# Optimization experiments

Measured on AMD Instinct MI355X. Metric: run time of the kernel, lower is better.

The kernel has to match this reference:

```python
import jax, jax.numpy as jnp
import numpy as np

D_MODEL = 1024
K_QUERY = 32
K_TOPK = 4

def setup_inputs() -> dict:
    key = jax.random.key(0)
    k1, k2, k3, k4, k5 = jax.random.split(key, 5)
    x = jax.random.normal(k1, (4, 2048, D_MODEL), dtype=jnp.float32)
    # nn.Linear(d_model, k_query): weight [k_query, d_model], bias [k_query]
    sc = 1.0 / np.sqrt(D_MODEL)
    Wq = jax.random.uniform(k2, (K_QUERY, D_MODEL), jnp.float32, -sc, sc)
    bq = jax.random.uniform(k3, (K_QUERY,), jnp.float32, -sc, sc)
    Wk = jax.random.uniform(k4, (K_QUERY, D_MODEL), jnp.float32, -sc, sc)
    bk = jax.random.uniform(k5, (K_QUERY,), jnp.float32, -sc, sc)
    return {"x": x, "Wq": Wq, "bq": bq, "Wk": Wk, "bk": bk}

def reference(x, Wq, bq, Wk, bk):
    # x: [B, T, D]
    queries = jnp.einsum('btd,kd->btk', x, Wq) + bq      # [B, T, Kq]
    keys = jnp.einsum('btd,kd->btk', x, Wk) + bk         # [B, T, Kq]
    sim = jnp.einsum('btk,bsk->bts', queries, keys)      # [B, T, T]
    sim = sim / jnp.sqrt(jnp.float32(queries.shape[-1]))
    _, topk_idx = jax.lax.top_k(sim, K_TOPK)              # [B, T, K]
    # gather neighbors per (b, t): x[b, topk_idx[b, t]] -> [B, T, K, D]
    neighbors = jax.vmap(lambda xb, ib: xb[ib])(x, topk_idx)
    gathered = neighbors.mean(axis=2)                     # [B, T, D]
    return gathered
```

## Files before the change

kernel.cpp:

```cpp
#include <hip/hip_runtime.h>
#include <math.h>

#define D_MODEL 1024
#define T_SEQ   2048
#define NBATCH  4
#define NROWS   (NBATCH * T_SEQ)
#define NOUT    64
#define NQTR    4

#define SKLD 264
#define SQLD 36
#define XLD  1032

typedef double v4df __attribute__((ext_vector_type(4)));

__device__ __forceinline__ bool key_gt(float av, int ai, float bv, int bi) {
    return (av > bv) || (av == bv && ai < bi);
}

__device__ __forceinline__ void cmpswap(float& v0, int& i0, float& v1, int& i1) {
    bool sw = key_gt(v1, i1, v0, i0);
    float nv0 = sw ? v1 : v0, nv1 = sw ? v0 : v1;
    int   ni0 = sw ? i1 : i0, ni1 = sw ? i0 : i1;
    v0 = nv0; v1 = nv1; i0 = ni0; i1 = ni1;
}

__device__ __forceinline__ void merge4(float (&a)[4], int (&ai)[4],
                                       float b0, int j0, float b1, int j1,
                                       float b2, int j2, float b3, int j3) {
    if (!key_gt(a[0], ai[0], b3, j3)) { a[0] = b3; ai[0] = j3; }
    if (!key_gt(a[1], ai[1], b2, j2)) { a[1] = b2; ai[1] = j2; }
    if (!key_gt(a[2], ai[2], b1, j1)) { a[2] = b1; ai[2] = j1; }
    if (!key_gt(a[3], ai[3], b0, j0)) { a[3] = b0; ai[3] = j0; }
    cmpswap(a[0], ai[0], a[2], ai[2]);
    cmpswap(a[1], ai[1], a[3], ai[3]);
    cmpswap(a[0], ai[0], a[1], ai[1]);
    cmpswap(a[2], ai[2], a[3], ai[3]);
}

__device__ __forceinline__ void insert4(float (&tv)[4], int (&tix)[4], float v, int idx) {
    if (v > tv[3]) {
        bool g0 = v > tv[0], g1 = v > tv[1], g2 = v > tv[2];
        float n0 = g0 ? v : tv[0];
        int   m0 = g0 ? idx : tix[0];
        float n1 = g1 ? (g0 ? tv[0] : v) : tv[1];
        int   m1 = g1 ? (g0 ? tix[0] : idx) : tix[1];
        float n2 = g2 ? (g1 ? tv[1] : v) : tv[2];
        int   m2 = g2 ? (g1 ? tix[1] : idx) : tix[2];
        float n3 = g2 ? tv[2] : v;
        int   m3 = g2 ? tix[2] : idx;
        tv[0] = n0; tv[1] = n1; tv[2] = n2; tv[3] = n3;
        tix[0] = m0; tix[1] = m1; tix[2] = m2; tix[3] = m3;
    }
}

__global__ __launch_bounds__(64) void mfma_probe(int* __restrict__ tab)
{
    __shared__ double Aref[16][4];
    __shared__ double Bref[4][16];
    __shared__ double Dref[16][16];

    const int lane = threadIdx.x;
    {
        const int m = lane & 15, k = lane >> 4;
        Aref[m][k] = (double)(1 + m * 4 + k);
        Bref[k][m] = (double)(1 + k * 16 + m);
    }
    __syncthreads();
    for (int e = lane; e < 256; e += 64) {
        const int m = e >> 4, n = e & 15;
        double s = 0.0;
        for (int k = 0; k < 4; ++k) s += Aref[m][k] * Bref[k][n];
        Dref[m][n] = s;
    }
    __syncthreads();

    int found = -1;
    for (int h = 0; h < 16; ++h) {
        if (found >= 0) break;
        const int fa = h & 1, fb = (h >> 1) & 1, fd = h >> 2;
        const int am = fa ? (lane >> 2) : (lane & 15);
        const int ak = fa ? (lane & 3)  : (lane >> 4);
        const int bn = fb ? (lane >> 2) : (lane & 15);
        const int bk = fb ? (lane & 3)  : (lane >> 4);
        v4df c = {0.0, 0.0, 0.0, 0.0};
        c = __builtin_amdgcn_mfma_f64_16x16x4f64(Aref[am][ak], Bref[bk][bn], c, 0, 0, 0);
        bool ok = true;
        #pragma unroll
        for (int i = 0; i < 4; ++i) {
            int dm, dn;
            if (fd == 0)      { dm = 4 * (lane >> 4) + i; dn = lane & 15; }
            else if (fd == 1) { dn = 4 * (lane >> 4) + i; dm = lane & 15; }
            else if (fd == 2) { dm = (lane >> 4) + 4 * i; dn = lane & 15; }
            else              { dn = (lane >> 4) + 4 * i; dm = lane & 15; }
            if (c[i] != Dref[dm][dn]) ok = false;
        }
        if (__all(ok)) found = h;
    }

    const int fa = (found >= 0) ? (found & 1) : 0;
    const int fb = (found >= 0) ? ((found >> 1) & 1) : 0;
    const int fd = (found >= 0) ? (found >> 2) : 0;
    tab[1   + lane] = fa ? (lane >> 2) : (lane & 15);
    tab[65  + lane] = fa ? (lane & 3)  : (lane >> 4);
    tab[129 + lane] = fb ? (lane & 3)  : (lane >> 4);
    tab[193 + lane] = fb ? (lane >> 2) : (lane & 15);
    #pragma unroll
    for (int i = 0; i < 4; ++i) {
        int dm, dn;
        if (fd == 0)      { dm = 4 * (lane >> 4) + i; dn = lane & 15; }
        else if (fd == 1) { dn = 4 * (lane >> 4) + i; dm = lane & 15; }
        else if (fd == 2) { dm = (lane >> 4) + 4 * i; dn = lane & 15; }
        else              { dn = (lane >> 4) + 4 * i; dm = lane & 15; }
        tab[257 + lane * 4 + i] = dm;
        tab[513 + lane * 4 + i] = dn;
    }
    if (lane == 0) tab[0] = found;
}

__global__ __launch_bounds__(256) void wprep_kernel(
    const float* __restrict__ Wq, const float* __restrict__ Wk,
    double* __restrict__ Wdt)
{
    const int idx = blockIdx.x * 256 + threadIdx.x;
    const int o = idx & 63;
    const int d = idx >> 6;
    float v = (o < 32) ? Wq[(size_t)o * D_MODEL + d]
                       : Wk[(size_t)(o - 32) * D_MODEL + d];
    Wdt[(size_t)d * 64 + o] = (double)v;
}

__global__ __launch_bounds__(512) void proj_mfma(
    const float* __restrict__ x, const double* __restrict__ Wdt,
    const float* __restrict__ bq, const float* __restrict__ bk_,
    const int* __restrict__ tab,
    float* __restrict__ Qt, float* __restrict__ Kt)
{
    __shared__ float  xlds[16 * XLD];
    __shared__ double comb[4][64][4];

    const int tid  = threadIdx.x;
    const int lane = tid & 63;
    const int wav  = tid >> 6;
    const int og   = __builtin_amdgcn_readfirstlane(wav >> 1);
    const int half = __builtin_amdgcn_readfirstlane(wav & 1);
    const int row0 = blockIdx.x * 16;
    const int dbase = half * 512;

    const int flag = tab[0];
    const int am  = tab[1   + lane];
    const int ak  = tab[65  + lane];
    const int bkk = tab[129 + lane];
    const int bn  = tab[193 + lane];

    const double* wcol = Wdt + og * 16;

    #pragma unroll
    for (int j = 0; j < 8; ++j) {
        const int f  = j * 512 + tid;
        const int r  = f >> 8;
        const int c4 = f & 255;
        float4 v = *reinterpret_cast<const float4*>(
            x + (size_t)(row0 + r) * D_MODEL + c4 * 4);
        *reinterpret_cast<float4*>(&xlds[r * XLD + c4 * 4]) = v;
    }
    __syncthreads();

    v4df acc = {0.0, 0.0, 0.0, 0.0};

    if (flag >= 0) {
        #pragma unroll 8
        for (int kk = 0; kk < 128; ++kk) {
            double a = (double)xlds[am * XLD + dbase + kk * 4 + ak];
            double b = wcol[(size_t)(dbase + kk * 4 + bkk) * 64 + bn];
            acc = __builtin_amdgcn_mfma_f64_16x16x4f64(a, b, acc, 0, 0, 0);
        }
    } else {
        const int n  = lane & 15;
        const int r4 = (lane >> 4) * 4;
        for (int dd = 0; dd < 512; ++dd) {
            const int d = dbase + dd;
            double wv = wcol[(size_t)d * 64 + n];
            #pragma unroll
            for (int i = 0; i < 4; ++i)
                acc[i] = fma((double)xlds[(r4 + i) * XLD + d], wv, acc[i]);
        }
    }

    if (half == 1) {
        #pragma unroll
        for (int i = 0; i < 4; ++i) comb[og][lane][i] = acc[i];
    }
    __syncthreads();

    if (half == 0) {
        #pragma unroll
        for (int i = 0; i < 4; ++i) {
            const double tot = acc[i] + comb[og][lane][i];
            const int dmv = tab[257 + lane * 4 + i];
            const int dnv = tab[513 + lane * 4 + i];
            const int out = og * 16 + dnv;
            const int row = row0 + dmv;
            const int bb  = row >> 11, t = row & 2047;
            const double bias = (out < 32) ? (double)bq[out] : (double)bk_[out - 32];
            const float v = (float)(tot + bias);
            if (out < 32) Qt[((size_t)bb * 32 + out) * T_SEQ + t] = v;
            else          Kt[((size_t)bb * 32 + (out - 32)) * T_SEQ + t] = v;
        }
    }
}

__global__ __launch_bounds__(256) void sim_topk(
    const float* __restrict__ Qt, const float* __restrict__ Kt,
    float* __restrict__ candVal ,
    int*   __restrict__ candIdx )
{
    __shared__ float klds[32 * SKLD];
    __shared__ float qlds[32 * SQLD];
    __shared__ float cV[4][32][4];
    __shared__ int   cI[4][32][4];

    const int tid  = threadIdx.x;
    const int lane = tid & 63;
    const int wav  = tid >> 6;
    const int qtr  = blockIdx.x & 3;
    const int tt   = (blockIdx.x >> 2) & 63;
    const int b    = blockIdx.x >> 8;
    const int tblk = tt * 32;
    const int sq0  = qtr * 512;

    const float* QtB = Qt + (size_t)b * 32 * T_SEQ;
    const float* KtB = Kt + (size_t)b * 32 * T_SEQ;

    {
        const int i  = tid >> 3;
        const int t4 = (tid & 7) * 4;
        float4 v = *reinterpret_cast<const float4*>(QtB + (size_t)i * T_SEQ + tblk + t4);
        *reinterpret_cast<float4*>(&qlds[i * SQLD + t4]) = v;
    }

    const int t0 = (tid & 7) * 4;
    const int s0 = (tid >> 3) * 8;

    float tv[4][4]; int tix[4][4];
    #pragma unroll
    for (int r = 0; r < 4; ++r)
        #pragma unroll
        for (int j = 0; j < 4; ++j) { tv[r][j] = -INFINITY; tix[r][j] = 0x7fffffff; }

    for (int st = 0; st < 2; ++st) {
        __syncthreads();
        #pragma unroll
        for (int j = 0; j < 8; ++j) {
            const int f  = (tid + j * 256) * 4;
            const int ki = f >> 8;
            const int ks = f & 255;
            float4 v = *reinterpret_cast<const float4*>(
                KtB + (size_t)ki * T_SEQ + sq0 + st * 256 + ks);
            *reinterpret_cast<float4*>(&klds[ki * SKLD + ks]) = v;
        }
        __syncthreads();

        float acc[4][8];
        #pragma unroll
        for (int r = 0; r < 4; ++r)
            #pragma unroll
            for (int c = 0; c < 8; ++c) acc[r][c] = 0.f;

        #pragma unroll 4
        for (int i = 0; i < 32; ++i) {
            float4 qv  = *reinterpret_cast<const float4*>(&qlds[i * SQLD + t0]);
            float4 kv0 = *reinterpret_cast<const float4*>(&klds[i * SKLD + s0]);
            float4 kv1 = *reinterpret_cast<const float4*>(&klds[i * SKLD + s0 + 4]);
            const float qa[4] = {qv.x, qv.y, qv.z, qv.w};
            const float ka[8] = {kv0.x, kv0.y, kv0.z, kv0.w, kv1.x, kv1.y, kv1.z, kv1.w};
            #pragma unroll
            for (int r = 0; r < 4; ++r)
                #pragma unroll
                for (int c = 0; c < 8; ++c)
                    acc[r][c] = fmaf(qa[r], ka[c], acc[r][c]);
        }

        const int sbase = sq0 + st * 256 + s0;
        #pragma unroll
        for (int c = 0; c < 8; ++c)
            #pragma unroll
            for (int r = 0; r < 4; ++r)
                insert4(tv[r], tix[r], acc[r][c], sbase + c);
    }

    #pragma unroll
    for (int m = 8; m <= 32; m <<= 1) {
        #pragma unroll
        for (int r = 0; r < 4; ++r) {
            float b0 = __shfl_xor(tv[r][0], m, 64);
            float b1 = __shfl_xor(tv[r][1], m, 64);
            float b2 = __shfl_xor(tv[r][2], m, 64);
            float b3 = __shfl_xor(tv[r][3], m, 64);
            int   j0 = __shfl_xor(tix[r][0], m, 64);
            int   j1 = __shfl_xor(tix[r][1], m, 64);
            int   j2 = __shfl_xor(tix[r][2], m, 64);
            int   j3 = __shfl_xor(tix[r][3], m, 64);
            merge4(tv[r], tix[r], b0, j0, b1, j1, b2, j2, b3, j3);
        }
    }

    if (lane < 8) {
        #pragma unroll
        for (int r = 0; r < 4; ++r)
            #pragma unroll
            for (int j = 0; j < 4; ++j) {
                cV[wav][lane * 4 + r][j] = tv[r][j];
                cI[wav][lane * 4 + r][j] = tix[r][j];
            }
    }
    __syncthreads();

    if (tid < 32) {
        float mv[4]; int mi[4];
        #pragma unroll
        for (int j = 0; j < 4; ++j) { mv[j] = cV[0][tid][j]; mi[j] = cI[0][tid][j]; }
        #pragma unroll
        for (int w = 1; w < 4; ++w)
            merge4(mv, mi,
                   cV[w][tid][0], cI[w][tid][0],
                   cV[w][tid][1], cI[w][tid][1],
                   cV[w][tid][2], cI[w][tid][2],
                   cV[w][tid][3], cI[w][tid][3]);
        const size_t row = (size_t)b * T_SEQ + tblk + tid;
        float4 vv = {mv[0], mv[1], mv[2], mv[3]};
        int4   ii = {mi[0], mi[1], mi[2], mi[3]};
        *reinterpret_cast<float4*>(candVal + ((size_t)qtr * NROWS + row) * 4) = vv;
        *reinterpret_cast<int4*>(candIdx + ((size_t)qtr * NROWS + row) * 4) = ii;
    }
}

__global__ __launch_bounds__(256) void merge_gather(
    const float* __restrict__ x,
    const float* __restrict__ candVal, const int* __restrict__ candIdx,
    float* __restrict__ out)
{
    __shared__ int topIdx[8][4];

    const int tid  = threadIdx.x;
    const int row0 = blockIdx.x * 8;
    const int b    = row0 >> 11;

    if (tid < 8) {
        const size_t row = row0 + tid;
        float4 v0 = *reinterpret_cast<const float4*>(candVal + row * 4);
        int4   i0 = *reinterpret_cast<const int4*>(candIdx + row * 4);
        float mv[4] = {v0.x, v0.y, v0.z, v0.w};
        int   mi[4] = {i0.x, i0.y, i0.z, i0.w};
        #pragma unroll
        for (int q = 1; q < NQTR; ++q) {
            float4 v1 = *reinterpret_cast<const float4*>(candVal + ((size_t)q * NROWS + row) * 4);
            int4   i1 = *reinterpret_cast<const int4*>(candIdx + ((size_t)q * NROWS + row) * 4);
            merge4(mv, mi, v1.x, i1.x, v1.y, i1.y, v1.z, i1.z, v1.w, i1.w);
        }
        #pragma unroll
        for (int j = 0; j < 4; ++j) topIdx[tid][j] = mi[j];
    }
    __syncthreads();

    const float* xb = x + (size_t)b * T_SEQ * D_MODEL;
    float* ob = out + (size_t)row0 * D_MODEL;
    #pragma unroll
    for (int r = 0; r < 8; ++r) {
        const int i0 = topIdx[r][0], i1 = topIdx[r][1], i2 = topIdx[r][2], i3 = topIdx[r][3];
        float4 a0 = *(reinterpret_cast<const float4*>(xb + (size_t)i0 * D_MODEL) + tid);
        float4 a1 = *(reinterpret_cast<const float4*>(xb + (size_t)i1 * D_MODEL) + tid);
        float4 a2 = *(reinterpret_cast<const float4*>(xb + (size_t)i2 * D_MODEL) + tid);
        float4 a3 = *(reinterpret_cast<const float4*>(xb + (size_t)i3 * D_MODEL) + tid);
        float4 o;
        o.x = (a0.x + a1.x + a2.x + a3.x) * 0.25f;
        o.y = (a0.y + a1.y + a2.y + a3.y) * 0.25f;
        o.z = (a0.z + a1.z + a2.z + a3.z) * 0.25f;
        o.w = (a0.w + a1.w + a2.w + a3.w) * 0.25f;
        *(reinterpret_cast<float4*>(ob + (size_t)r * D_MODEL) + tid) = o;
    }
}

extern "C" void kernel_launch(void* const* d_in, const int* in_sizes, int n_in,
                              void* d_out, int out_size, void* d_ws, size_t ws_size,
                              hipStream_t stream) {
    const float* x  = (const float*)d_in[0];
    const float* Wq = (const float*)d_in[1];
    const float* bq = (const float*)d_in[2];
    const float* Wk = (const float*)d_in[3];
    const float* bk = (const float*)d_in[4];
    float* out = (float*)d_out;

    char* wsb = (char*)d_ws;
    int*    tab  = (int*)wsb;
    double* Wdt  = (double*)(wsb + 4096);
    float*  Qt   = (float*)(wsb + 4096 + (size_t)D_MODEL * NOUT * 8);
    float*  Kt   = Qt + (size_t)NBATCH * 32 * T_SEQ;
    float*  candVal = (float*)((char*)Kt + (size_t)NBATCH * 32 * T_SEQ * 4);
    int*    candIdx = (int*)((char*)candVal + (size_t)NQTR * NROWS * 4 * 4);

    mfma_probe<<<dim3(1), dim3(64), 0, stream>>>(tab);
    wprep_kernel<<<dim3(256), dim3(256), 0, stream>>>(Wq, Wk, Wdt);
    proj_mfma<<<dim3(NROWS / 16), dim3(512), 0, stream>>>(x, Wdt, bq, bk, tab, Qt, Kt);
    sim_topk<<<dim3(1024), dim3(256), 0, stream>>>(Qt, Kt, candVal, candIdx);
    merge_gather<<<dim3(1024), dim3(256), 0, stream>>>(x, candVal, candIdx, out);
}
```

Measured before the change: 163.9 us.

## Compute similarity scores with FP64 MFMA and split keys into halves

Replaces the FP32 FMA-based similarity/top-k kernel with one that uses the 16x16x4 f64 MFMA, relying on the probed lane layout table to map accumulator elements back to rows and columns. Each block now handles 16 query rows against half of the keys, with each wave covering 256 keys, so only two candidate partitions need merging in the gather kernel. K and Q fragments are loaded directly from global memory instead of staging through LDS. The aim is to cut ALU time in the dominant kernel and make the tie ordering match the higher-precision reference. The cost is FP64 conversion overhead, uncoalesced strided global loads and extra shuffle reductions.

```diff
diff --git a/kernel.cpp b/kernel.cpp
--- a/kernel.cpp
+++ b/kernel.cpp
@@ -6,10 +6,7 @@
 #define NBATCH  4
 #define NROWS   (NBATCH * T_SEQ)
 #define NOUT    64
-#define NQTR    4
-
-#define SKLD 264
-#define SQLD 36
+
 #define XLD  1032
 
 typedef double v4df __attribute__((ext_vector_type(4)));
@@ -54,6 +51,18 @@
     }
 }
 
+__device__ __forceinline__ void bfly_merge(float (&tv)[4], int (&tix)[4], int m) {
+    float b0 = __shfl_xor(tv[0], m, 64);
+    float b1 = __shfl_xor(tv[1], m, 64);
+    float b2 = __shfl_xor(tv[2], m, 64);
+    float b3 = __shfl_xor(tv[3], m, 64);
+    int   j0 = __shfl_xor(tix[0], m, 64);
+    int   j1 = __shfl_xor(tix[1], m, 64);
+    int   j2 = __shfl_xor(tix[2], m, 64);
+    int   j3 = __shfl_xor(tix[3], m, 64);
+    merge4(tv, tix, b0, j0, b1, j1, b2, j2, b3, j3);
+}
+
 __global__ __launch_bounds__(64) void mfma_probe(int* __restrict__ tab)
 {
     __shared__ double Aref[16][4];
@@ -210,37 +219,44 @@
     }
 }
 
-__global__ __launch_bounds__(256) void sim_topk(
+__global__ __launch_bounds__(256) void sim_mfma(
     const float* __restrict__ Qt, const float* __restrict__ Kt,
+    const int* __restrict__ tab,
     float* __restrict__ candVal ,
     int*   __restrict__ candIdx )
 {
-    __shared__ float klds[32 * SKLD];
-    __shared__ float qlds[32 * SQLD];
-    __shared__ float cV[4][32][4];
-    __shared__ int   cI[4][32][4];
+    __shared__ float cV[4][16][4];
+    __shared__ int   cI[4][16][4];
 
     const int tid  = threadIdx.x;
     const int lane = tid & 63;
-    const int wav  = tid >> 6;
-    const int qtr  = blockIdx.x & 3;
-    const int tt   = (blockIdx.x >> 2) & 63;
+    const int wav  = __builtin_amdgcn_readfirstlane(tid >> 6);
+    const int half = blockIdx.x & 1;
+    const int tt   = (blockIdx.x >> 1) & 127;
     const int b    = blockIdx.x >> 8;
-    const int tblk = tt * 32;
-    const int sq0  = qtr * 512;
+    const int trow0 = tt * 16;
+    const int sbase0 = half * 1024 + wav * 256;
 
     const float* QtB = Qt + (size_t)b * 32 * T_SEQ;
     const float* KtB = Kt + (size_t)b * 32 * T_SEQ;
 
-    {
-        const int i  = tid >> 3;
-        const int t4 = (tid & 7) * 4;
-        float4 v = *reinterpret_cast<const float4*>(QtB + (size_t)i * T_SEQ + tblk + t4);
-        *reinterpret_cast<float4*>(&qlds[i * SQLD + t4]) = v;
-    }
-
-    const int t0 = (tid & 7) * 4;
-    const int s0 = (tid >> 3) * 8;
+    const int flag = tab[0];
+    const int am  = tab[1   + lane];
+    const int ak  = tab[65  + lane];
+    const int bkk = tab[129 + lane];
+    const int bn  = tab[193 + lane];
+    int dmv[4], dnv[4];
+    #pragma unroll
+    for (int i = 0; i < 4; ++i) {
+        dmv[i] = tab[257 + lane * 4 + i];
+        dnv[i] = tab[513 + lane * 4 + i];
+    }
+    const bool modeB = __builtin_amdgcn_readfirstlane((int)(dmv[0] == dmv[1])) != 0;
+
+    double a[8];
+    #pragma unroll
+    for (int c = 0; c < 8; ++c)
+        a[c] = (double)QtB[(size_t)(4 * c + ak) * T_SEQ + trow0 + am];
 
     float tv[4][4]; int tix[4][4];
     #pragma unroll
@@ -248,75 +264,84 @@
         #pragma unroll
         for (int j = 0; j < 4; ++j) { tv[r][j] = -INFINITY; tix[r][j] = 0x7fffffff; }
 
-    for (int st = 0; st < 2; ++st) {
-        __syncthreads();
-        #pragma unroll
-        for (int j = 0; j < 8; ++j) {
-            const int f  = (tid + j * 256) * 4;
-            const int ki = f >> 8;
-            const int ks = f & 255;
-            float4 v = *reinterpret_cast<const float4*>(
-                KtB + (size_t)ki * T_SEQ + sq0 + st * 256 + ks);
-            *reinterpret_cast<float4*>(&klds[ki * SKLD + ks]) = v;
-        }
-        __syncthreads();
-
-        float acc[4][8];
-        #pragma unroll
-        for (int r = 0; r < 4; ++r)
-            #pragma unroll
-            for (int c = 0; c < 8; ++c) acc[r][c] = 0.f;
-
-        #pragma unroll 4
-        for (int i = 0; i < 32; ++i) {
-            float4 qv  = *reinterpret_cast<const float4*>(&qlds[i * SQLD + t0]);
-            float4 kv0 = *reinterpret_cast<const float4*>(&klds[i * SKLD + s0]);
-            float4 kv1 = *reinterpret_cast<const float4*>(&klds[i * SKLD + s0 + 4]);
-            const float qa[4] = {qv.x, qv.y, qv.z, qv.w};
-            const float ka[8] = {kv0.x, kv0.y, kv0.z, kv0.w, kv1.x, kv1.y, kv1.z, kv1.w};
-            #pragma unroll
-            for (int r = 0; r < 4; ++r)
+    for (int pp = 0; pp < 8; ++pp) {
+        const int sb0 = sbase0 + pp * 32;
+        const int sb1 = sb0 + 16;
+        v4df acc0 = {0.0, 0.0, 0.0, 0.0};
+        v4df acc1 = {0.0, 0.0, 0.0, 0.0};
+
+        if (flag >= 0) {
+            double b0[8], b1[8];
+            #pragma unroll
+            for (int c = 0; c < 8; ++c) {
+                b0[c] = (double)KtB[(size_t)(4 * c + bkk) * T_SEQ + sb0 + bn];
+                b1[c] = (double)KtB[(size_t)(4 * c + bkk) * T_SEQ + sb1 + bn];
+            }
+            #pragma unroll
+            for (int c = 0; c < 8; ++c) {
+                acc0 = __builtin_amdgcn_mfma_f64_16x16x4f64(a[c], b0[c], acc0, 0, 0, 0);
+                acc1 = __builtin_amdgcn_mfma_f64_16x16x4f64(a[c], b1[c], acc1, 0, 0, 0);
+            }
+        } else {
+            #pragma unroll
+            for (int i = 0; i < 4; ++i) {
+                double s0 = 0.0, s1 = 0.0;
+                for (int k = 0; k < 32; ++k) {
+                    double q = (double)QtB[(size_t)k * T_SEQ + trow0 + dmv[i]];
+                    s0 = fma(q, (double)KtB[(size_t)k * T_SEQ + sb0 + dnv[i]], s0);
+                    s1 = fma(q, (double)KtB[(size_t)k * T_SEQ + sb1 + dnv[i]], s1);
+                }
+                acc0[i] = s0; acc1[i] = s1;
+            }
+        }
+
+        if (!modeB) {
+            #pragma unroll
+            for (int i = 0; i < 4; ++i) {
+                insert4(tv[i], tix[i], (float)acc0[i], sb0 + dnv[i]);
+                insert4(tv[i], tix[i], (float)acc1[i], sb1 + dnv[i]);
+            }
+        } else {
+            #pragma unroll
+            for (int i = 0; i < 4; ++i) {
+                insert4(tv[0], tix[0], (float)acc0[i], sb0 + dnv[i]);
+                insert4(tv[0], tix[0], (float)acc1[i], sb1 + dnv[i]);
+            }
+        }
+    }
+
+    if (!modeB) {
+        bfly_merge(tv[0], tix[0], 1); bfly_merge(tv[0], tix[0], 2);
+        bfly_merge(tv[0], tix[0], 4); bfly_merge(tv[0], tix[0], 8);
+        bfly_merge(tv[1], tix[1], 1); bfly_merge(tv[1], tix[1], 2);
+        bfly_merge(tv[1], tix[1], 4); bfly_merge(tv[1], tix[1], 8);
+        bfly_merge(tv[2], tix[2], 1); bfly_merge(tv[2], tix[2], 2);
+        bfly_merge(tv[2], tix[2], 4); bfly_merge(tv[2], tix[2], 8);
+        bfly_merge(tv[3], tix[3], 1); bfly_merge(tv[3], tix[3], 2);
+        bfly_merge(tv[3], tix[3], 4); bfly_merge(tv[3], tix[3], 8);
+        if ((lane & 15) == 0) {
+            #pragma unroll
+            for (int i = 0; i < 4; ++i)
                 #pragma unroll
-                for (int c = 0; c < 8; ++c)
-                    acc[r][c] = fmaf(qa[r], ka[c], acc[r][c]);
-        }
-
-        const int sbase = sq0 + st * 256 + s0;
-        #pragma unroll
-        for (int c = 0; c < 8; ++c)
-            #pragma unroll
-            for (int r = 0; r < 4; ++r)
-                insert4(tv[r], tix[r], acc[r][c], sbase + c);
-    }
-
-    #pragma unroll
-    for (int m = 8; m <= 32; m <<= 1) {
-        #pragma unroll
-        for (int r = 0; r < 4; ++r) {
-            float b0 = __shfl_xor(tv[r][0], m, 64);
-            float b1 = __shfl_xor(tv[r][1], m, 64);
-            float b2 = __shfl_xor(tv[r][2], m, 64);
-            float b3 = __shfl_xor(tv[r][3], m, 64);
-            int   j0 = __shfl_xor(tix[r][0], m, 64);
-            int   j1 = __shfl_xor(tix[r][1], m, 64);
-            int   j2 = __shfl_xor(tix[r][2], m, 64);
-            int   j3 = __shfl_xor(tix[r][3], m, 64);
-            merge4(tv[r], tix[r], b0, j0, b1, j1, b2, j2, b3, j3);
-        }
-    }
-
-    if (lane < 8) {
-        #pragma unroll
-        for (int r = 0; r < 4; ++r)
+                for (int j = 0; j < 4; ++j) {
+                    cV[wav][dmv[i]][j] = tv[i][j];
+                    cI[wav][dmv[i]][j] = tix[i][j];
+                }
+        }
+    } else {
+        bfly_merge(tv[0], tix[0], 16);
+        bfly_merge(tv[0], tix[0], 32);
+        if (lane < 16) {
             #pragma unroll
             for (int j = 0; j < 4; ++j) {
-                cV[wav][lane * 4 + r][j] = tv[r][j];
-                cI[wav][lane * 4 + r][j] = tix[r][j];
-            }
-    }
-    __syncthreads();
-
-    if (tid < 32) {
+                cV[wav][lane][j] = tv[0][j];
+                cI[wav][lane][j] = tix[0][j];
+            }
+        }
+    }
+    __syncthreads();
+
+    if (tid < 16) {
         float mv[4]; int mi[4];
         #pragma unroll
         for (int j = 0; j < 4; ++j) { mv[j] = cV[0][tid][j]; mi[j] = cI[0][tid][j]; }
@@ -327,11 +352,11 @@
                    cV[w][tid][1], cI[w][tid][1],
                    cV[w][tid][2], cI[w][tid][2],
                    cV[w][tid][3], cI[w][tid][3]);
-        const size_t row = (size_t)b * T_SEQ + tblk + tid;
+        const size_t row = (size_t)b * T_SEQ + trow0 + tid;
         float4 vv = {mv[0], mv[1], mv[2], mv[3]};
         int4   ii = {mi[0], mi[1], mi[2], mi[3]};
-        *reinterpret_cast<float4*>(candVal + ((size_t)qtr * NROWS + row) * 4) = vv;
-        *reinterpret_cast<int4*>(candIdx + ((size_t)qtr * NROWS + row) * 4) = ii;
+        *reinterpret_cast<float4*>(candVal + ((size_t)half * NROWS + row) * 4) = vv;
+        *reinterpret_cast<int4*>(candIdx + ((size_t)half * NROWS + row) * 4) = ii;
     }
 }
 
@@ -350,14 +375,11 @@
         const size_t row = row0 + tid;
         float4 v0 = *reinterpret_cast<const float4*>(candVal + row * 4);
         int4   i0 = *reinterpret_cast<const int4*>(candIdx + row * 4);
+        float4 v1 = *reinterpret_cast<const float4*>(candVal + ((size_t)NROWS + row) * 4);
+        int4   i1 = *reinterpret_cast<const int4*>(candIdx + ((size_t)NROWS + row) * 4);
         float mv[4] = {v0.x, v0.y, v0.z, v0.w};
         int   mi[4] = {i0.x, i0.y, i0.z, i0.w};
-        #pragma unroll
-        for (int q = 1; q < NQTR; ++q) {
-            float4 v1 = *reinterpret_cast<const float4*>(candVal + ((size_t)q * NROWS + row) * 4);
-            int4   i1 = *reinterpret_cast<const int4*>(candIdx + ((size_t)q * NROWS + row) * 4);
-            merge4(mv, mi, v1.x, i1.x, v1.y, i1.y, v1.z, i1.z, v1.w, i1.w);
-        }
+        merge4(mv, mi, v1.x, i1.x, v1.y, i1.y, v1.z, i1.z, v1.w, i1.w);
         #pragma unroll
         for (int j = 0; j < 4; ++j) topIdx[tid][j] = mi[j];
     }
@@ -397,11 +419,11 @@
     float*  Qt   = (float*)(wsb + 4096 + (size_t)D_MODEL * NOUT * 8);
     float*  Kt   = Qt + (size_t)NBATCH * 32 * T_SEQ;
     float*  candVal = (float*)((char*)Kt + (size_t)NBATCH * 32 * T_SEQ * 4);
-    int*    candIdx = (int*)((char*)candVal + (size_t)NQTR * NROWS * 4 * 4);
+    int*    candIdx = (int*)((char*)candVal + (size_t)2 * NROWS * 4 * 4);
 
     mfma_probe<<<dim3(1), dim3(64), 0, stream>>>(tab);
     wprep_kernel<<<dim3(256), dim3(256), 0, stream>>>(Wq, Wk, Wdt);
     proj_mfma<<<dim3(NROWS / 16), dim3(512), 0, stream>>>(x, Wdt, bq, bk, tab, Qt, Kt);
-    sim_topk<<<dim3(1024), dim3(256), 0, stream>>>(Qt, Kt, candVal, candIdx);
+    sim_mfma<<<dim3(1024), dim3(256), 0, stream>>>(Qt, Kt, tab, candVal, candIdx);
     merge_gather<<<dim3(1024), dim3(256), 0, stream>>>(x, candVal, candIdx, out);
 }
```

After: 211.5 us. +29.0%, slower.

## Inline MFMA layout probe and pre-swizzle W and x into fragment order

Applied to the files above, without the earlier changes.

Removes the separate probe kernel and its lookup table; each wave now runs the f64 MFMA layout probe inline with register-computed references. W is written in per-lane MFMA fragment order so B operands load with coalesced stride-64 accesses, and x is staged into LDS in fragment order so A operands are contiguous per lane. This drops one kernel launch and the strided W loads and table reads, at the cost of repeating the probe in every block and loading x with scalar strided global reads instead of float4.

```diff
diff --git a/kernel.cpp b/kernel.cpp
--- a/kernel.cpp
+++ b/kernel.cpp
@@ -10,7 +10,6 @@
 
 #define SKLD 264
 #define SQLD 36
-#define XLD  1032
 
 typedef double v4df __attribute__((ext_vector_type(4)));
 
@@ -54,37 +53,21 @@
     }
 }
 
-__global__ __launch_bounds__(64) void mfma_probe(int* __restrict__ tab)
-{
-    __shared__ double Aref[16][4];
-    __shared__ double Bref[4][16];
-    __shared__ double Dref[16][16];
-
-    const int lane = threadIdx.x;
-    {
-        const int m = lane & 15, k = lane >> 4;
-        Aref[m][k] = (double)(1 + m * 4 + k);
-        Bref[k][m] = (double)(1 + k * 16 + m);
-    }
-    __syncthreads();
-    for (int e = lane; e < 256; e += 64) {
-        const int m = e >> 4, n = e & 15;
-        double s = 0.0;
-        for (int k = 0; k < 4; ++k) s += Aref[m][k] * Bref[k][n];
-        Dref[m][n] = s;
-    }
-    __syncthreads();
-
+__device__ __forceinline__ void probe_f64(int lane, int& flag,
+                                          int& am, int& ak, int& bkk, int& bn,
+                                          int (&dmv)[4], int (&dnv)[4]) {
     int found = -1;
     for (int h = 0; h < 16; ++h) {
         if (found >= 0) break;
         const int fa = h & 1, fb = (h >> 1) & 1, fd = h >> 2;
-        const int am = fa ? (lane >> 2) : (lane & 15);
-        const int ak = fa ? (lane & 3)  : (lane >> 4);
-        const int bn = fb ? (lane >> 2) : (lane & 15);
-        const int bk = fb ? (lane & 3)  : (lane >> 4);
+        const int tam = fa ? (lane >> 2) : (lane & 15);
+        const int tak = fa ? (lane & 3)  : (lane >> 4);
+        const int tbn = fb ? (lane >> 2) : (lane & 15);
+        const int tbk = fb ? (lane & 3)  : (lane >> 4);
+        const double a = (double)(1 + tam * 4 + tak);
+        const double b = (double)(1 + tbk * 16 + tbn);
         v4df c = {0.0, 0.0, 0.0, 0.0};
-        c = __builtin_amdgcn_mfma_f64_16x16x4f64(Aref[am][ak], Bref[bk][bn], c, 0, 0, 0);
+        c = __builtin_amdgcn_mfma_f64_16x16x4f64(a, b, c, 0, 0, 0);
         bool ok = true;
         #pragma unroll
         for (int i = 0; i < 4; ++i) {
@@ -93,50 +76,55 @@
             else if (fd == 1) { dn = 4 * (lane >> 4) + i; dm = lane & 15; }
             else if (fd == 2) { dm = (lane >> 4) + 4 * i; dn = lane & 15; }
             else              { dn = (lane >> 4) + 4 * i; dm = lane & 15; }
-            if (c[i] != Dref[dm][dn]) ok = false;
+            double ref = 0.0;
+            #pragma unroll
+            for (int k = 0; k < 4; ++k)
+                ref += (double)((1 + 4 * dm + k) * (1 + 16 * k + dn));
+            if (c[i] != ref) ok = false;
         }
         if (__all(ok)) found = h;
     }
-
+    flag = found;
     const int fa = (found >= 0) ? (found & 1) : 0;
     const int fb = (found >= 0) ? ((found >> 1) & 1) : 0;
     const int fd = (found >= 0) ? (found >> 2) : 0;
-    tab[1   + lane] = fa ? (lane >> 2) : (lane & 15);
-    tab[65  + lane] = fa ? (lane & 3)  : (lane >> 4);
-    tab[129 + lane] = fb ? (lane & 3)  : (lane >> 4);
-    tab[193 + lane] = fb ? (lane >> 2) : (lane & 15);
+    am  = fa ? (lane >> 2) : (lane & 15);
+    ak  = fa ? (lane & 3)  : (lane >> 4);
+    bn  = fb ? (lane >> 2) : (lane & 15);
+    bkk = fb ? (lane & 3)  : (lane >> 4);
     #pragma unroll
     for (int i = 0; i < 4; ++i) {
-        int dm, dn;
-        if (fd == 0)      { dm = 4 * (lane >> 4) + i; dn = lane & 15; }
-        else if (fd == 1) { dn = 4 * (lane >> 4) + i; dm = lane & 15; }
-        else if (fd == 2) { dm = (lane >> 4) + 4 * i; dn = lane & 15; }
-        else              { dn = (lane >> 4) + 4 * i; dm = lane & 15; }
-        tab[257 + lane * 4 + i] = dm;
-        tab[513 + lane * 4 + i] = dn;
-    }
-    if (lane == 0) tab[0] = found;
+        if (fd == 0)      { dmv[i] = 4 * (lane >> 4) + i; dnv[i] = lane & 15; }
+        else if (fd == 1) { dnv[i] = 4 * (lane >> 4) + i; dmv[i] = lane & 15; }
+        else if (fd == 2) { dmv[i] = (lane >> 4) + 4 * i; dnv[i] = lane & 15; }
+        else              { dnv[i] = (lane >> 4) + 4 * i; dmv[i] = lane & 15; }
+    }
 }
 
 __global__ __launch_bounds__(256) void wprep_kernel(
     const float* __restrict__ Wq, const float* __restrict__ Wk,
-    double* __restrict__ Wdt)
+    double* __restrict__ Wfrag)
 {
-    const int idx = blockIdx.x * 256 + threadIdx.x;
-    const int o = idx & 63;
-    const int d = idx >> 6;
-    float v = (o < 32) ? Wq[(size_t)o * D_MODEL + d]
-                       : Wk[(size_t)(o - 32) * D_MODEL + d];
-    Wdt[(size_t)d * 64 + o] = (double)v;
+    const int lane = threadIdx.x & 63;
+    int flag, am, ak, bkk, bn, dmv[4], dnv[4];
+    probe_f64(lane, flag, am, ak, bkk, bn, dmv, dnv);
+
+    const int g  = blockIdx.x * 256 + threadIdx.x;
+    const int kk = (g >> 6) & 255;
+    const int og = g >> 14;
+    const int o  = og * 16 + bn;
+    const int d  = kk * 4 + bkk;
+    const float v = (o < 32) ? Wq[(size_t)o * D_MODEL + d]
+                             : Wk[(size_t)(o - 32) * D_MODEL + d];
+    Wfrag[((size_t)og * 256 + kk) * 64 + lane] = (double)v;
 }
 
 __global__ __launch_bounds__(512) void proj_mfma(
-    const float* __restrict__ x, const double* __restrict__ Wdt,
+    const float* __restrict__ x, const double* __restrict__ Wfrag,
     const float* __restrict__ bq, const float* __restrict__ bk_,
-    const int* __restrict__ tab,
     float* __restrict__ Qt, float* __restrict__ Kt)
 {
-    __shared__ float  xlds[16 * XLD];
+    __shared__ float  aFrag[256 * 64];
     __shared__ double comb[4][64][4];
 
     const int tid  = threadIdx.x;
@@ -145,45 +133,41 @@
     const int og   = __builtin_amdgcn_readfirstlane(wav >> 1);
     const int half = __builtin_amdgcn_readfirstlane(wav & 1);
     const int row0 = blockIdx.x * 16;
-    const int dbase = half * 512;
-
-    const int flag = tab[0];
-    const int am  = tab[1   + lane];
-    const int ak  = tab[65  + lane];
-    const int bkk = tab[129 + lane];
-    const int bn  = tab[193 + lane];
-
-    const double* wcol = Wdt + og * 16;
-
-    #pragma unroll
-    for (int j = 0; j < 8; ++j) {
-        const int f  = j * 512 + tid;
-        const int r  = f >> 8;
-        const int c4 = f & 255;
-        float4 v = *reinterpret_cast<const float4*>(
-            x + (size_t)(row0 + r) * D_MODEL + c4 * 4);
-        *reinterpret_cast<float4*>(&xlds[r * XLD + c4 * 4]) = v;
+
+    int flag, am, ak, bkk, bn, dmv[4], dnv[4];
+    probe_f64(lane, flag, am, ak, bkk, bn, dmv, dnv);
+    (void)bkk; (void)bn;
+
+    {
+        const float* xr = x + (size_t)(row0 + am) * D_MODEL + ak;
+        #pragma unroll 8
+        for (int kq = 0; kq < 32; ++kq) {
+            const int kk = wav * 32 + kq;
+            aFrag[kk * 64 + lane] = xr[kk * 4];
+        }
     }
     __syncthreads();
 
     v4df acc = {0.0, 0.0, 0.0, 0.0};
 
     if (flag >= 0) {
+        const double* wf = Wfrag + ((size_t)og * 256 + half * 128) * 64 + lane;
+        const float*  af = aFrag + half * 128 * 64 + lane;
         #pragma unroll 8
         for (int kk = 0; kk < 128; ++kk) {
-            double a = (double)xlds[am * XLD + dbase + kk * 4 + ak];
-            double b = wcol[(size_t)(dbase + kk * 4 + bkk) * 64 + bn];
+            double a = (double)af[kk * 64];
+            double b = wf[(size_t)kk * 64];
             acc = __builtin_amdgcn_mfma_f64_16x16x4f64(a, b, acc, 0, 0, 0);
         }
     } else {
         const int n  = lane & 15;
         const int r4 = (lane >> 4) * 4;
         for (int dd = 0; dd < 512; ++dd) {
-            const int d = dbase + dd;
-            double wv = wcol[(size_t)d * 64 + n];
+            const int d = half * 512 + dd;
+            const double wv = Wfrag[((size_t)og * 256 + (d >> 2)) * 64 + (((d & 3) << 4) | n)];
             #pragma unroll
             for (int i = 0; i < 4; ++i)
-                acc[i] = fma((double)xlds[(r4 + i) * XLD + d], wv, acc[i]);
+                acc[i] = fma((double)aFrag[(d >> 2) * 64 + (((d & 3) << 4) | (r4 + i))], wv, acc[i]);
         }
     }
 
@@ -197,10 +181,8 @@
         #pragma unroll
         for (int i = 0; i < 4; ++i) {
             const double tot = acc[i] + comb[og][lane][i];
-            const int dmv = tab[257 + lane * 4 + i];
-            const int dnv = tab[513 + lane * 4 + i];
-            const int out = og * 16 + dnv;
-            const int row = row0 + dmv;
+            const int out = og * 16 + dnv[i];
+            const int row = row0 + dmv[i];
             const int bb  = row >> 11, t = row & 2047;
             const double bias = (out < 32) ? (double)bq[out] : (double)bk_[out - 32];
             const float v = (float)(tot + bias);
@@ -392,16 +374,14 @@
     float* out = (float*)d_out;
 
     char* wsb = (char*)d_ws;
-    int*    tab  = (int*)wsb;
-    double* Wdt  = (double*)(wsb + 4096);
-    float*  Qt   = (float*)(wsb + 4096 + (size_t)D_MODEL * NOUT * 8);
-    float*  Kt   = Qt + (size_t)NBATCH * 32 * T_SEQ;
+    double* Wfrag = (double*)wsb;
+    float*  Qt    = (float*)(wsb + (size_t)4 * 256 * 64 * 8);
+    float*  Kt    = Qt + (size_t)NBATCH * 32 * T_SEQ;
     float*  candVal = (float*)((char*)Kt + (size_t)NBATCH * 32 * T_SEQ * 4);
     int*    candIdx = (int*)((char*)candVal + (size_t)NQTR * NROWS * 4 * 4);
 
-    mfma_probe<<<dim3(1), dim3(64), 0, stream>>>(tab);
-    wprep_kernel<<<dim3(256), dim3(256), 0, stream>>>(Wq, Wk, Wdt);
-    proj_mfma<<<dim3(NROWS / 16), dim3(512), 0, stream>>>(x, Wdt, bq, bk, tab, Qt, Kt);
+    wprep_kernel<<<dim3(256), dim3(256), 0, stream>>>(Wq, Wk, Wfrag);
+    proj_mfma<<<dim3(NROWS / 16), dim3(512), 0, stream>>>(x, Wfrag, bq, bk, Qt, Kt);
     sim_topk<<<dim3(1024), dim3(256), 0, stream>>>(Qt, Kt, candVal, candIdx);
     merge_gather<<<dim3(1024), dim3(256), 0, stream>>>(x, candVal, candIdx, out);
 }
```

New measurement: 175.0 us. 1.07x slower.
